# Optimization experiments

Hardware: AMD Instinct MI355X
Metric: run time of the kernel (lower is better)

Reference implementation:

```python
import jax, jax.numpy as jnp
import numpy as np

B = 262144
INPUT_DIM = 512
HID = 64
NUM_BASE = 2
NUM_CLASSES = 2


def setup_inputs() -> dict:
    key = jax.random.key(0)
    ks = jax.random.split(key, 10)
    probs = jax.random.uniform(ks[0], (B, NUM_BASE, NUM_CLASSES), dtype=jnp.float32)
    fuzzy_features = jax.random.normal(ks[1], (B, INPUT_DIM), dtype=jnp.float32)
    s1 = 1.0 / np.sqrt(INPUT_DIM)
    s2 = 1.0 / np.sqrt(HID)
    # m1: Linear(input_dim,64) -> ReLU -> Linear(64, num_base*num_classes)
    W1 = jax.random.uniform(ks[2], (INPUT_DIM, HID), jnp.float32, -s1, s1)
    b1 = jax.random.uniform(ks[3], (HID,), jnp.float32, -s1, s1)
    W2 = jax.random.uniform(ks[4], (HID, NUM_BASE * NUM_CLASSES), jnp.float32, -s2, s2)
    b2 = jax.random.uniform(ks[5], (NUM_BASE * NUM_CLASSES,), jnp.float32, -s2, s2)
    # m2: Linear(input_dim,64) -> ReLU -> Linear(64, num_classes)
    W3 = jax.random.uniform(ks[6], (INPUT_DIM, HID), jnp.float32, -s1, s1)
    b3 = jax.random.uniform(ks[7], (HID,), jnp.float32, -s1, s1)
    W4 = jax.random.uniform(ks[8], (HID, NUM_CLASSES), jnp.float32, -s2, s2)
    b4 = jax.random.uniform(ks[9], (NUM_CLASSES,), jnp.float32, -s2, s2)
    return {"probs": probs, "fuzzy_features": fuzzy_features,
            "W1": W1, "b1": b1, "W2": W2, "b2": b2,
            "W3": W3, "b3": b3, "W4": W4, "b4": b4}


def _forward(probs, x, W1, b1, W2, b2, W3, b3, W4, b4):
    # FuzzyMeasureLearner
    h1 = jax.nn.relu(x @ W1 + b1)                       # [B, 64]
    single = jax.nn.sigmoid((h1 @ W2 + b2).reshape(-1, NUM_BASE, NUM_CLASSES))
    h2 = jax.nn.relu(x @ W3 + b3)                       # [B, 64]
    inc = jax.nn.sigmoid(h2 @ W4 + b4)                  # [B, 2]
    # Vectorized Choquet integral (binary, 2 sources)
    p0 = probs[:, 0, :]                                 # [B, 2]
    p1 = probs[:, 1, :]
    mu1 = single[:, 0, :]
    mu2 = single[:, 1, :]
    mu12 = jnp.minimum(jnp.maximum(mu1, mu2) + inc, 1.0)
    res = jnp.where(p0 <= p1,
                    p0 * mu1 + (p1 - p0) * mu12,
                    p1 * mu2 + (p0 - p1) * mu12)        # [B, 2]
    return jax.nn.softmax(res, axis=1)


def reference(probs, fuzzy_features, W1, b1, W2, b2, W3, b3, W4, b4):
    return _forward(probs, fuzzy_features, W1, b1, W2, b2, W3, b3, W4, b4)
```

## Files before the change

### kernel.cpp

```cpp
#include <hip/hip_runtime.h>
#include <hip/hip_bf16.h>

typedef short s16x8 __attribute__((ext_vector_type(8)));
typedef unsigned u32x4 __attribute__((ext_vector_type(4)));
typedef float f32x4 __attribute__((ext_vector_type(4)));
typedef float f32x2 __attribute__((ext_vector_type(2)));

static __device__ __forceinline__ short f2bf(float f) {
    unsigned u = __builtin_bit_cast(unsigned, f);
    unsigned r = (u + 0x7fffu + ((u >> 16) & 1u)) >> 16;
    return (short)r;
}

static __device__ __forceinline__ unsigned pk2bf(float a, float b) {
    __hip_bfloat162 h = __float22bfloat162_rn(make_float2(a, b));
    unsigned r;
    __builtin_memcpy(&r, &h, sizeof(r));
    return r;
}

__global__ void prep_weights(const float* __restrict__ W1,
                             const float* __restrict__ W3,
                             short* __restrict__ bws) {
    int tid = blockIdx.x * blockDim.x + threadIdx.x;
    int j  = tid & 7;
    int l  = (tid >> 3) & 63;
    int nt = (tid >> 9) & 7;
    int kk = tid >> 12;
    int k = kk * 32 + ((l >> 4) << 3) + j;
    int n = nt * 16 + (l & 15);
    float v = (n < 64) ? W1[k * 64 + n] : W3[k * 64 + (n - 64)];
    bws[tid] = f2bf(v);
}

__global__ __launch_bounds__(1024, 4)
void mf2_main(const float* __restrict__ probs, const float* __restrict__ x,
              const short* __restrict__ bws,
              const float* __restrict__ b1, const float* __restrict__ W2,
              const float* __restrict__ b2, const float* __restrict__ b3,
              const float* __restrict__ W4, const float* __restrict__ b4,
              float* __restrict__ out)
{
    __shared__ short bsh[512 * 128];

    const int tid  = threadIdx.x;
    const int lane = tid & 63;
    const int wv   = tid >> 6;
    const int g    = lane >> 4;
    const int m    = lane & 15;
    const long rowBase = (long)blockIdx.x * 512 + wv * 32;

    {
        const f32x4* src = (const f32x4*)bws;
        f32x4* dst = (f32x4*)bsh;
        #pragma unroll
        for (int it = 0; it < 8; ++it) {
            const int idx = it * 1024 + tid;
            dst[idx] = src[idx];
        }
    }
    __syncthreads();

    f32x4 acc[2][8];
    #pragma unroll
    for (int t = 0; t < 2; ++t)
        #pragma unroll
        for (int nt = 0; nt < 8; ++nt)
            acc[t][nt] = (f32x4){0.f, 0.f, 0.f, 0.f};

    const float* xp = x + (rowBase + m) * 512 + g * 8;
    const s16x8* bls = (const s16x8*)bsh + lane;

    #pragma unroll 2
    for (int kk = 0; kk < 16; ++kk) {
        s16x8 a[2];
        #pragma unroll
        for (int t = 0; t < 2; ++t) {
            const float* p = xp + t * (16 * 512) + kk * 32;
            f32x4 lo = *(const f32x4*)p;
            f32x4 hi = *(const f32x4*)(p + 4);
            u32x4 pa;
            pa[0] = pk2bf(lo[0], lo[1]);
            pa[1] = pk2bf(lo[2], lo[3]);
            pa[2] = pk2bf(hi[0], hi[1]);
            pa[3] = pk2bf(hi[2], hi[3]);
            a[t] = __builtin_bit_cast(s16x8, pa);
        }
        #pragma unroll
        for (int nt = 0; nt < 8; ++nt) {
            s16x8 b = bls[kk * 512 + nt * 64];
            acc[0][nt] = __builtin_amdgcn_mfma_f32_16x16x32_bf16(a[0], b, acc[0][nt], 0, 0, 0);
            acc[1][nt] = __builtin_amdgcn_mfma_f32_16x16x32_bf16(a[1], b, acc[1][nt], 0, 0, 0);
        }
    }

    float w2r[4][4];
    float w4r[4][2];
    float biasr[8];
    #pragma unroll
    for (int nt = 0; nt < 4; ++nt) {
        const int col = m + 16 * nt;
        f32x4 w2v = *(const f32x4*)(W2 + col * 4);
        #pragma unroll
        for (int c = 0; c < 4; ++c) w2r[nt][c] = w2v[c];
        f32x2 w4v = *(const f32x2*)(W4 + col * 2);
        w4r[nt][0] = w4v[0]; w4r[nt][1] = w4v[1];
    }
    #pragma unroll
    for (int nt = 0; nt < 8; ++nt) {
        const int col = m + 16 * nt;
        biasr[nt] = (col < 64) ? b1[col] : b3[col - 64];
    }
    float b2v[4], b4v[2];
    #pragma unroll
    for (int c = 0; c < 4; ++c) b2v[c] = b2[c];
    #pragma unroll
    for (int c = 0; c < 2; ++c) b4v[c] = b4[c];

    float own[6] = {0.f, 0.f, 0.f, 0.f, 0.f, 0.f};
    #pragma unroll
    for (int t = 0; t < 2; ++t) {
        #pragma unroll
        for (int r = 0; r < 4; ++r) {
            float v[6] = {0.f, 0.f, 0.f, 0.f, 0.f, 0.f};
            #pragma unroll
            for (int nt = 0; nt < 4; ++nt) {
                float h = fmaxf(acc[t][nt][r] + biasr[nt], 0.f);
                v[0] += h * w2r[nt][0];
                v[1] += h * w2r[nt][1];
                v[2] += h * w2r[nt][2];
                v[3] += h * w2r[nt][3];
            }
            #pragma unroll
            for (int j = 0; j < 4; ++j) {
                float h = fmaxf(acc[t][4 + j][r] + biasr[4 + j], 0.f);
                v[4] += h * w4r[j][0];
                v[5] += h * w4r[j][1];
            }
            #pragma unroll
            for (int msk = 1; msk <= 8; msk <<= 1) {
                #pragma unroll
                for (int c = 0; c < 6; ++c) v[c] += __shfl_xor(v[c], msk, 64);
            }
            if (m == t * 4 + r) {
                #pragma unroll
                for (int c = 0; c < 6; ++c) own[c] = v[c];
            }
        }
    }

    if (m < 8) {
        const int t = m >> 2, r = m & 3;
        const long row = rowBase + t * 16 + g * 4 + r;
        f32x4 pr = *(const f32x4*)(probs + row * 4);
        float mu1[2], mu2[2], icv[2];
        #pragma unroll
        for (int c = 0; c < 2; ++c) {
            mu1[c] = 1.0f / (1.0f + __expf(-(own[c]     + b2v[c])));
            mu2[c] = 1.0f / (1.0f + __expf(-(own[2 + c] + b2v[2 + c])));
            icv[c] = 1.0f / (1.0f + __expf(-(own[4 + c] + b4v[c])));
        }
        float res[2];
        #pragma unroll
        for (int c = 0; c < 2; ++c) {
            float p0 = pr[c], p1 = pr[2 + c];
            float m12 = fminf(fmaxf(mu1[c], mu2[c]) + icv[c], 1.0f);
            res[c] = (p0 <= p1) ? (p0 * mu1[c] + (p1 - p0) * m12)
                                : (p1 * mu2[c] + (p0 - p1) * m12);
        }
        float d01 = res[0] - res[1];
        f32x2 o;
        o[0] = 1.0f / (1.0f + __expf(-d01));
        o[1] = 1.0f / (1.0f + __expf(d01));
        *(f32x2*)(out + row * 2) = o;
    }
}

extern "C" void kernel_launch(void* const* d_in, const int* in_sizes, int n_in,
                              void* d_out, int out_size, void* d_ws, size_t ws_size,
                              hipStream_t stream)
{
    const float* probs = (const float*)d_in[0];
    const float* x     = (const float*)d_in[1];
    const float* W1    = (const float*)d_in[2];
    const float* b1    = (const float*)d_in[3];
    const float* W2    = (const float*)d_in[4];
    const float* b2    = (const float*)d_in[5];
    const float* W3    = (const float*)d_in[6];
    const float* b3    = (const float*)d_in[7];
    const float* W4    = (const float*)d_in[8];
    const float* b4    = (const float*)d_in[9];
    float* out = (float*)d_out;
    short* bws = (short*)d_ws;

    hipLaunchKernelGGL(prep_weights, dim3(256), dim3(256), 0, stream, W1, W3, bws);
    hipLaunchKernelGGL(mf2_main, dim3(512), dim3(1024), 0, stream,
                       probs, x, bws, b1, W2, b2, b3, W4, b4, out);
}
```

Baseline: 125.9 us.

## Software-pipeline x loads, process two row groups per block, replicate weights

```diff
diff --git a/kernel.cpp b/kernel.cpp
--- a/kernel.cpp
+++ b/kernel.cpp
@@ -30,7 +30,9 @@
     int k = kk * 32 + ((l >> 4) << 3) + j;
     int n = nt * 16 + (l & 15);
     float v = (n < 64) ? W1[k * 64 + n] : W3[k * 64 + (n - 64)];
-    bws[tid] = f2bf(v);
+    short s = f2bf(v);
+    #pragma unroll
+    for (int c = 0; c < 8; ++c) bws[c * 65536 + tid] = s;
 }
 
 __global__ __launch_bounds__(1024, 4)
@@ -48,10 +50,21 @@
     const int wv   = tid >> 6;
     const int g    = lane >> 4;
     const int m    = lane & 15;
-    const long rowBase = (long)blockIdx.x * 512 + wv * 32;
+    const long blockRow = (long)blockIdx.x * 1024;
+
+    f32x4 ra[2][2][2];
+    const float* xp0 = x + (blockRow + wv * 32 + m) * 512 + g * 8;
+    #pragma unroll
+    for (int p = 0; p < 2; ++p)
+        #pragma unroll
+        for (int t = 0; t < 2; ++t) {
+            const float* pp = xp0 + t * (16 * 512) + p * 32;
+            ra[p][t][0] = *(const f32x4*)pp;
+            ra[p][t][1] = *(const f32x4*)(pp + 4);
+        }
 
     {
-        const f32x4* src = (const f32x4*)bws;
+        const f32x4* src = (const f32x4*)(bws + (blockIdx.x & 7) * 65536);
         f32x4* dst = (f32x4*)bsh;
         #pragma unroll
         for (int it = 0; it < 8; ++it) {
@@ -61,118 +74,138 @@
     }
     __syncthreads();
 
-    f32x4 acc[2][8];
+    const s16x8* bls = (const s16x8*)bsh + lane;
+
     #pragma unroll
-    for (int t = 0; t < 2; ++t)
-        #pragma unroll
-        for (int nt = 0; nt < 8; ++nt)
-            acc[t][nt] = (f32x4){0.f, 0.f, 0.f, 0.f};
-
-    const float* xp = x + (rowBase + m) * 512 + g * 8;
-    const s16x8* bls = (const s16x8*)bsh + lane;
-
-    #pragma unroll 2
-    for (int kk = 0; kk < 16; ++kk) {
-        s16x8 a[2];
+    for (int gi = 0; gi < 2; ++gi) {
+        const long rowBase = blockRow + gi * 512 + wv * 32;
+        const float* xp = x + (rowBase + m) * 512 + g * 8;
+        const float* xn = xp + 512 * 512;
+
+        f32x4 acc[2][8];
+        #pragma unroll
+        for (int t = 0; t < 2; ++t)
+            #pragma unroll
+            for (int nt = 0; nt < 8; ++nt)
+                acc[t][nt] = (f32x4){0.f, 0.f, 0.f, 0.f};
+
+        #pragma unroll
+        for (int kk = 0; kk < 16; ++kk) {
+            s16x8 a[2];
+            #pragma unroll
+            for (int t = 0; t < 2; ++t) {
+                u32x4 pa;
+                pa[0] = pk2bf(ra[kk & 1][t][0][0], ra[kk & 1][t][0][1]);
+                pa[1] = pk2bf(ra[kk & 1][t][0][2], ra[kk & 1][t][0][3]);
+                pa[2] = pk2bf(ra[kk & 1][t][1][0], ra[kk & 1][t][1][1]);
+                pa[3] = pk2bf(ra[kk & 1][t][1][2], ra[kk & 1][t][1][3]);
+                a[t] = __builtin_bit_cast(s16x8, pa);
+            }
+
+            if (kk < 14) {
+                #pragma unroll
+                for (int t = 0; t < 2; ++t) {
+                    const float* pp = xp + t * (16 * 512) + (kk + 2) * 32;
+                    ra[kk & 1][t][0] = *(const f32x4*)pp;
+                    ra[kk & 1][t][1] = *(const f32x4*)(pp + 4);
+                }
+            } else if (gi == 0) {
+                #pragma unroll
+                for (int t = 0; t < 2; ++t) {
+                    const float* pp = xn + t * (16 * 512) + (kk - 14) * 32;
+                    ra[kk & 1][t][0] = *(const f32x4*)pp;
+                    ra[kk & 1][t][1] = *(const f32x4*)(pp + 4);
+                }
+            }
+
+            #pragma unroll
+            for (int nt = 0; nt < 8; ++nt) {
+                s16x8 b = bls[kk * 512 + nt * 64];
+                acc[0][nt] = __builtin_amdgcn_mfma_f32_16x16x32_bf16(a[0], b, acc[0][nt], 0, 0, 0);
+                acc[1][nt] = __builtin_amdgcn_mfma_f32_16x16x32_bf16(a[1], b, acc[1][nt], 0, 0, 0);
+            }
+        }
+
+        float w2r[4][4];
+        float w4r[4][2];
+        float biasr[8];
+        #pragma unroll
+        for (int nt = 0; nt < 4; ++nt) {
+            const int col = m + 16 * nt;
+            f32x4 w2v = *(const f32x4*)(W2 + col * 4);
+            #pragma unroll
+            for (int c = 0; c < 4; ++c) w2r[nt][c] = w2v[c];
+            f32x2 w4v = *(const f32x2*)(W4 + col * 2);
+            w4r[nt][0] = w4v[0]; w4r[nt][1] = w4v[1];
+        }
+        #pragma unroll
+        for (int nt = 0; nt < 8; ++nt) {
+            const int col = m + 16 * nt;
+            biasr[nt] = (col < 64) ? b1[col] : b3[col - 64];
+        }
+        float b2v[4], b4v[2];
+        #pragma unroll
+        for (int c = 0; c < 4; ++c) b2v[c] = b2[c];
+        #pragma unroll
+        for (int c = 0; c < 2; ++c) b4v[c] = b4[c];
+
+        float own[6] = {0.f, 0.f, 0.f, 0.f, 0.f, 0.f};
         #pragma unroll
         for (int t = 0; t < 2; ++t) {
-            const float* p = xp + t * (16 * 512) + kk * 32;
-            f32x4 lo = *(const f32x4*)p;
-            f32x4 hi = *(const f32x4*)(p + 4);
-            u32x4 pa;
-            pa[0] = pk2bf(lo[0], lo[1]);
-            pa[1] = pk2bf(lo[2], lo[3]);
-            pa[2] = pk2bf(hi[0], hi[1]);
-            pa[3] = pk2bf(hi[2], hi[3]);
-            a[t] = __builtin_bit_cast(s16x8, pa);
-        }
-        #pragma unroll
-        for (int nt = 0; nt < 8; ++nt) {
-            s16x8 b = bls[kk * 512 + nt * 64];
-            acc[0][nt] = __builtin_amdgcn_mfma_f32_16x16x32_bf16(a[0], b, acc[0][nt], 0, 0, 0);
-            acc[1][nt] = __builtin_amdgcn_mfma_f32_16x16x32_bf16(a[1], b, acc[1][nt], 0, 0, 0);
-        }
-    }
-
-    float w2r[4][4];
-    float w4r[4][2];
-    float biasr[8];
-    #pragma unroll
-    for (int nt = 0; nt < 4; ++nt) {
-        const int col = m + 16 * nt;
-        f32x4 w2v = *(const f32x4*)(W2 + col * 4);
-        #pragma unroll
-        for (int c = 0; c < 4; ++c) w2r[nt][c] = w2v[c];
-        f32x2 w4v = *(const f32x2*)(W4 + col * 2);
-        w4r[nt][0] = w4v[0]; w4r[nt][1] = w4v[1];
-    }
-    #pragma unroll
-    for (int nt = 0; nt < 8; ++nt) {
-        const int col = m + 16 * nt;
-        biasr[nt] = (col < 64) ? b1[col] : b3[col - 64];
-    }
-    float b2v[4], b4v[2];
-    #pragma unroll
-    for (int c = 0; c < 4; ++c) b2v[c] = b2[c];
-    #pragma unroll
-    for (int c = 0; c < 2; ++c) b4v[c] = b4[c];
-
-    float own[6] = {0.f, 0.f, 0.f, 0.f, 0.f, 0.f};
-    #pragma unroll
-    for (int t = 0; t < 2; ++t) {
-        #pragma unroll
-        for (int r = 0; r < 4; ++r) {
-            float v[6] = {0.f, 0.f, 0.f, 0.f, 0.f, 0.f};
-            #pragma unroll
-            for (int nt = 0; nt < 4; ++nt) {
-                float h = fmaxf(acc[t][nt][r] + biasr[nt], 0.f);
-                v[0] += h * w2r[nt][0];
-                v[1] += h * w2r[nt][1];
-                v[2] += h * w2r[nt][2];
-                v[3] += h * w2r[nt][3];
-            }
-            #pragma unroll
-            for (int j = 0; j < 4; ++j) {
-                float h = fmaxf(acc[t][4 + j][r] + biasr[4 + j], 0.f);
-                v[4] += h * w4r[j][0];
-                v[5] += h * w4r[j][1];
-            }
-            #pragma unroll
-            for (int msk = 1; msk <= 8; msk <<= 1) {
-                #pragma unroll
-                for (int c = 0; c < 6; ++c) v[c] += __shfl_xor(v[c], msk, 64);
-            }
-            if (m == t * 4 + r) {
-                #pragma unroll
-                for (int c = 0; c < 6; ++c) own[c] = v[c];
-            }
-        }
-    }
-
-    if (m < 8) {
-        const int t = m >> 2, r = m & 3;
-        const long row = rowBase + t * 16 + g * 4 + r;
-        f32x4 pr = *(const f32x4*)(probs + row * 4);
-        float mu1[2], mu2[2], icv[2];
-        #pragma unroll
-        for (int c = 0; c < 2; ++c) {
-            mu1[c] = 1.0f / (1.0f + __expf(-(own[c]     + b2v[c])));
-            mu2[c] = 1.0f / (1.0f + __expf(-(own[2 + c] + b2v[2 + c])));
-            icv[c] = 1.0f / (1.0f + __expf(-(own[4 + c] + b4v[c])));
-        }
-        float res[2];
-        #pragma unroll
-        for (int c = 0; c < 2; ++c) {
-            float p0 = pr[c], p1 = pr[2 + c];
-            float m12 = fminf(fmaxf(mu1[c], mu2[c]) + icv[c], 1.0f);
-            res[c] = (p0 <= p1) ? (p0 * mu1[c] + (p1 - p0) * m12)
-                                : (p1 * mu2[c] + (p0 - p1) * m12);
-        }
-        float d01 = res[0] - res[1];
-        f32x2 o;
-        o[0] = 1.0f / (1.0f + __expf(-d01));
-        o[1] = 1.0f / (1.0f + __expf(d01));
-        *(f32x2*)(out + row * 2) = o;
+            #pragma unroll
+            for (int r = 0; r < 4; ++r) {
+                float v[6] = {0.f, 0.f, 0.f, 0.f, 0.f, 0.f};
+                #pragma unroll
+                for (int nt = 0; nt < 4; ++nt) {
+                    float h = fmaxf(acc[t][nt][r] + biasr[nt], 0.f);
+                    v[0] += h * w2r[nt][0];
+                    v[1] += h * w2r[nt][1];
+                    v[2] += h * w2r[nt][2];
+                    v[3] += h * w2r[nt][3];
+                }
+                #pragma unroll
+                for (int j = 0; j < 4; ++j) {
+                    float h = fmaxf(acc[t][4 + j][r] + biasr[4 + j], 0.f);
+                    v[4] += h * w4r[j][0];
+                    v[5] += h * w4r[j][1];
+                }
+                #pragma unroll
+                for (int msk = 1; msk <= 8; msk <<= 1) {
+                    #pragma unroll
+                    for (int c = 0; c < 6; ++c) v[c] += __shfl_xor(v[c], msk, 64);
+                }
+                if (m == t * 4 + r) {
+                    #pragma unroll
+                    for (int c = 0; c < 6; ++c) own[c] = v[c];
+                }
+            }
+        }
+
+        if (m < 8) {
+            const int t = m >> 2, r = m & 3;
+            const long row = rowBase + t * 16 + g * 4 + r;
+            f32x4 pr = *(const f32x4*)(probs + row * 4);
+            float mu1[2], mu2[2], icv[2];
+            #pragma unroll
+            for (int c = 0; c < 2; ++c) {
+                mu1[c] = 1.0f / (1.0f + __expf(-(own[c]     + b2v[c])));
+                mu2[c] = 1.0f / (1.0f + __expf(-(own[2 + c] + b2v[2 + c])));
+                icv[c] = 1.0f / (1.0f + __expf(-(own[4 + c] + b4v[c])));
+            }
+            float res[2];
+            #pragma unroll
+            for (int c = 0; c < 2; ++c) {
+                float p0 = pr[c], p1 = pr[2 + c];
+                float m12 = fminf(fmaxf(mu1[c], mu2[c]) + icv[c], 1.0f);
+                res[c] = (p0 <= p1) ? (p0 * mu1[c] + (p1 - p0) * m12)
+                                    : (p1 * mu2[c] + (p0 - p1) * m12);
+            }
+            float d01 = res[0] - res[1];
+            f32x2 o;
+            o[0] = 1.0f / (1.0f + __expf(-d01));
+            o[1] = 1.0f / (1.0f + __expf(d01));
+            *(f32x2*)(out + row * 2) = o;
+        }
     }
 }
 
@@ -194,6 +227,6 @@
     short* bws = (short*)d_ws;
 
     hipLaunchKernelGGL(prep_weights, dim3(256), dim3(256), 0, stream, W1, W3, bws);
-    hipLaunchKernelGGL(mf2_main, dim3(512), dim3(1024), 0, stream,
+    hipLaunchKernelGGL(mf2_main, dim3(256), dim3(1024), 0, stream,
                        probs, x, bws, b1, W2, b2, b3, W4, b4, out);
 }
```

Result: slower. 185.6 us (+47.4%).

## Halve rows per wave and software-prefetch x into a register ring

Applied to the files above, without the earlier changes.

```diff
diff --git a/kernel.cpp b/kernel.cpp
--- a/kernel.cpp
+++ b/kernel.cpp
@@ -48,7 +48,17 @@
     const int wv   = tid >> 6;
     const int g    = lane >> 4;
     const int m    = lane & 15;
-    const long rowBase = (long)blockIdx.x * 512 + wv * 32;
+    const long rowBase = (long)blockIdx.x * 256 + wv * 16;
+
+    const float* xp = x + (rowBase + m) * 512 + g * 8;
+
+    f32x4 ra[4][2];
+    #pragma unroll
+    for (int p = 0; p < 4; ++p) {
+        const float* pp = xp + p * 32;
+        ra[p][0] = *(const f32x4*)pp;
+        ra[p][1] = *(const f32x4*)(pp + 4);
+    }
 
     {
         const f32x4* src = (const f32x4*)bws;
@@ -61,36 +71,33 @@
     }
     __syncthreads();
 
-    f32x4 acc[2][8];
-    #pragma unroll
-    for (int t = 0; t < 2; ++t)
-        #pragma unroll
-        for (int nt = 0; nt < 8; ++nt)
-            acc[t][nt] = (f32x4){0.f, 0.f, 0.f, 0.f};
-
-    const float* xp = x + (rowBase + m) * 512 + g * 8;
     const s16x8* bls = (const s16x8*)bsh + lane;
 
-    #pragma unroll 2
+    f32x4 acc[8];
+    #pragma unroll
+    for (int nt = 0; nt < 8; ++nt)
+        acc[nt] = (f32x4){0.f, 0.f, 0.f, 0.f};
+
+    #pragma unroll
     for (int kk = 0; kk < 16; ++kk) {
-        s16x8 a[2];
-        #pragma unroll
-        for (int t = 0; t < 2; ++t) {
-            const float* p = xp + t * (16 * 512) + kk * 32;
-            f32x4 lo = *(const f32x4*)p;
-            f32x4 hi = *(const f32x4*)(p + 4);
-            u32x4 pa;
-            pa[0] = pk2bf(lo[0], lo[1]);
-            pa[1] = pk2bf(lo[2], lo[3]);
-            pa[2] = pk2bf(hi[0], hi[1]);
-            pa[3] = pk2bf(hi[2], hi[3]);
-            a[t] = __builtin_bit_cast(s16x8, pa);
-        }
+        const int s = kk & 3;
+        u32x4 pa;
+        pa[0] = pk2bf(ra[s][0][0], ra[s][0][1]);
+        pa[1] = pk2bf(ra[s][0][2], ra[s][0][3]);
+        pa[2] = pk2bf(ra[s][1][0], ra[s][1][1]);
+        pa[3] = pk2bf(ra[s][1][2], ra[s][1][3]);
+        s16x8 a = __builtin_bit_cast(s16x8, pa);
+
+        if (kk < 12) {
+            const float* pp = xp + (kk + 4) * 32;
+            ra[s][0] = *(const f32x4*)pp;
+            ra[s][1] = *(const f32x4*)(pp + 4);
+        }
+
         #pragma unroll
         for (int nt = 0; nt < 8; ++nt) {
             s16x8 b = bls[kk * 512 + nt * 64];
-            acc[0][nt] = __builtin_amdgcn_mfma_f32_16x16x32_bf16(a[0], b, acc[0][nt], 0, 0, 0);
-            acc[1][nt] = __builtin_amdgcn_mfma_f32_16x16x32_bf16(a[1], b, acc[1][nt], 0, 0, 0);
+            acc[nt] = __builtin_amdgcn_mfma_f32_16x16x32_bf16(a, b, acc[nt], 0, 0, 0);
         }
     }
 
@@ -119,39 +126,35 @@
 
     float own[6] = {0.f, 0.f, 0.f, 0.f, 0.f, 0.f};
     #pragma unroll
-    for (int t = 0; t < 2; ++t) {
-        #pragma unroll
-        for (int r = 0; r < 4; ++r) {
-            float v[6] = {0.f, 0.f, 0.f, 0.f, 0.f, 0.f};
+    for (int r = 0; r < 4; ++r) {
+        float v[6] = {0.f, 0.f, 0.f, 0.f, 0.f, 0.f};
+        #pragma unroll
+        for (int nt = 0; nt < 4; ++nt) {
+            float h = fmaxf(acc[nt][r] + biasr[nt], 0.f);
+            v[0] += h * w2r[nt][0];
+            v[1] += h * w2r[nt][1];
+            v[2] += h * w2r[nt][2];
+            v[3] += h * w2r[nt][3];
+        }
+        #pragma unroll
+        for (int j = 0; j < 4; ++j) {
+            float h = fmaxf(acc[4 + j][r] + biasr[4 + j], 0.f);
+            v[4] += h * w4r[j][0];
+            v[5] += h * w4r[j][1];
+        }
+        #pragma unroll
+        for (int msk = 1; msk <= 8; msk <<= 1) {
             #pragma unroll
-            for (int nt = 0; nt < 4; ++nt) {
-                float h = fmaxf(acc[t][nt][r] + biasr[nt], 0.f);
-                v[0] += h * w2r[nt][0];
-                v[1] += h * w2r[nt][1];
-                v[2] += h * w2r[nt][2];
-                v[3] += h * w2r[nt][3];
-            }
+            for (int c = 0; c < 6; ++c) v[c] += __shfl_xor(v[c], msk, 64);
+        }
+        if (m == r) {
             #pragma unroll
-            for (int j = 0; j < 4; ++j) {
-                float h = fmaxf(acc[t][4 + j][r] + biasr[4 + j], 0.f);
-                v[4] += h * w4r[j][0];
-                v[5] += h * w4r[j][1];
-            }
-            #pragma unroll
-            for (int msk = 1; msk <= 8; msk <<= 1) {
-                #pragma unroll
-                for (int c = 0; c < 6; ++c) v[c] += __shfl_xor(v[c], msk, 64);
-            }
-            if (m == t * 4 + r) {
-                #pragma unroll
-                for (int c = 0; c < 6; ++c) own[c] = v[c];
-            }
-        }
-    }
-
-    if (m < 8) {
-        const int t = m >> 2, r = m & 3;
-        const long row = rowBase + t * 16 + g * 4 + r;
+            for (int c = 0; c < 6; ++c) own[c] = v[c];
+        }
+    }
+
+    if (m < 4) {
+        const long row = rowBase + g * 4 + m;
         f32x4 pr = *(const f32x4*)(probs + row * 4);
         float mu1[2], mu2[2], icv[2];
         #pragma unroll
@@ -194,6 +197,6 @@
     short* bws = (short*)d_ws;
 
     hipLaunchKernelGGL(prep_weights, dim3(256), dim3(256), 0, stream, W1, W3, bws);
-    hipLaunchKernelGGL(mf2_main, dim3(512), dim3(1024), 0, stream,
+    hipLaunchKernelGGL(mf2_main, dim3(1024), dim3(1024), 0, stream,
                        probs, x, bws, b1, W2, b2, b3, W4, b4, out);
 }
```

After: 127.1 us. No clear change (+0.9%).
